# Optimization experiments

Measured on AMD Instinct MI355X. Metric: run time of the kernel, lower is better.

Reference implementation:

```python
import jax, jax.numpy as jnp
import numpy as np

GAMMA = 1.0
N_EXPERTS = 16
K = 8                      # number of trees (units of every Dense)
DEPTH = 4                  # log2(N_EXPERTS)
B, D_IN, D_OUT = 8192, 1024, 1024


def smoothstep(v):
    # 0 if v<=-g/2 ; 1 if v>=g/2 ; -2/g^3 v^3 + 3/(2g) v + 0.5 otherwise
    g = GAMMA
    poly = (-2.0 / g**3) * v**3 + (3.0 / (2.0 * g)) * v + 0.5
    return jnp.where(v <= -g / 2, 0.0, jnp.where(v >= g / 2, 1.0, poly))


def setup_inputs() -> dict:
    key = jax.random.key(0)
    ks = jax.random.split(key, 7)
    f = jax.random.normal(ks[0], (B, D_OUT, N_EXPERTS), jnp.float32)   # stacked experts
    x = jax.random.normal(ks[1], (B, D_IN), jnp.float32)               # routing inputs
    permutation_weights = jax.random.uniform(ks[2], (K, N_EXPERTS, N_EXPERTS), jnp.float32)
    zlo, zhi = -GAMMA / 100, GAMMA / 100                               # z_initializer range
    Wz = jax.random.uniform(ks[3], (N_EXPERTS - 1, D_IN, K), jnp.float32, zlo, zhi)
    bz = jax.random.uniform(ks[4], (N_EXPERTS - 1, K), jnp.float32, zlo, zhi)
    Ww = jax.random.uniform(ks[5], (N_EXPERTS, D_IN, K), jnp.float32)  # w_initializer U(0,1)
    bw = jax.random.uniform(ks[6], (N_EXPERTS, K), jnp.float32)
    return {"f": f, "x": x, "permutation_weights": permutation_weights,
            "Wz": Wz, "bz": bz, "Ww": Ww, "bw": bw}


def reference(f, x, permutation_weights, Wz, bz, Ww, bw):
    b = x.shape[0]
    # selector activations for all internal nodes (BFS order): [B, N_EXPERTS-1, K]
    s = smoothstep(jnp.einsum('bd,ndk->bnk', x, Wz) + bz)
    # propagate path probabilities level by level down the complete binary tree
    prob = jnp.ones((b, 1, K), x.dtype)
    for level in range(DEPTH):
        start = 2**level - 1
        p = s[:, start:start + 2**level, :]               # [B, 2^level, K]
        # left child gets prob*p, right child gets prob*(1-p)
        prob = jnp.stack([prob * p, prob * (1.0 - p)], axis=2).reshape(b, 2**(level + 1), K)
    # leaf dense outputs: [B, N_EXPERTS, K]
    a = jnp.einsum('bd,ndk->bnk', x, Ww) + bw
    log_prob = jnp.where(prob <= 0.0, jnp.finfo(jnp.float32).min, jnp.log(prob + 1e-8))
    s_bj = jnp.swapaxes(a + log_prob, 1, 2)               # [B, K, N_EXPERTS] (leaf order)
    g = jax.nn.softmax(s_bj.reshape(b, K * N_EXPERTS), axis=-1)
    g = g.reshape(b, 1, K, N_EXPERTS)                     # [B, 1, K, N]
    g_perm = jnp.einsum('bijk,jkl->bijl', g, permutation_weights)
    g_perm = jnp.sum(g_perm, axis=2, keepdims=True)       # [B, 1, 1, N]
    g_perm = g_perm / jnp.sum(g_perm, axis=-1, keepdims=True)
    # y = sum_n f[:, :, n] * g[:, n]  -> [B, D_OUT]
    y = jnp.einsum('bdn,bn->bd', f, g_perm[:, 0, 0, :])
    return y
```

## Files before the change

kernel.cpp:

```cpp
#include <hip/hip_runtime.h>
#include <hip/hip_bf16.h>
#include <math.h>

#define B_ROWS 8192
#define D_IN 1024
#define D_OUT 1024
#define NEXP 16
#define KDIM 8
#define NCOL 256

__global__ void wt_pack_kernel(const float* __restrict__ Wz,
                               const float* __restrict__ Ww,
                               float* __restrict__ Wt) {
    int d = blockIdx.x;
    int col = threadIdx.x;
    float v = 0.0f;
    if (col < 120) {
        int n = col >> 3, k = col & 7;
        v = Wz[n * (D_IN * 8) + d * 8 + k];
    } else if (col < 248) {
        int c = col - 120;
        int n = c >> 3, k = c & 7;
        v = Ww[n * (D_IN * 8) + d * 8 + k];
    }
    Wt[d * NCOL + col] = v;
}

#define BM 64
#define BN 64
#define KC 16
__global__ __launch_bounds__(256) void gemm_kernel(const float* __restrict__ x,
                                                   const float* __restrict__ Wt,
                                                   float* __restrict__ ZA) {
    __shared__ float xs[KC][BM];
    __shared__ float wsh[KC][BN];

    const int tid = threadIdx.x;
    const int bRow = blockIdx.x;
    const int bCol = blockIdx.y;
    const int tr = tid >> 4;
    const int tc = tid & 15;

    const int lxRow = tid >> 2;
    const int lxK = (tid & 3) << 2;
    const int lwK = tid >> 4;
    const int lwC = (tid & 15) << 2;

    const float* xg = x + (bRow * BM + lxRow) * D_IN + lxK;
    const float* wg = Wt + lwK * NCOL + bCol * BN + lwC;

    float4 px = *(const float4*)xg;
    float4 pw = *(const float4*)wg;

    float acc[4][4];
#pragma unroll
    for (int i = 0; i < 4; ++i)
#pragma unroll
        for (int j = 0; j < 4; ++j) acc[i][j] = 0.0f;

    for (int kc = 0; kc < D_IN; kc += KC) {
        xs[lxK + 0][lxRow] = px.x;
        xs[lxK + 1][lxRow] = px.y;
        xs[lxK + 2][lxRow] = px.z;
        xs[lxK + 3][lxRow] = px.w;
        *(float4*)&wsh[lwK][lwC] = pw;
        __syncthreads();
        if (kc + KC < D_IN) {
            px = *(const float4*)(xg + kc + KC);
            pw = *(const float4*)(wg + (kc + KC) * NCOL);
        }
#pragma unroll
        for (int kk = 0; kk < KC; ++kk) {
            const float4 xa = *(const float4*)&xs[kk][tr << 2];
            const float4 wv = *(const float4*)&wsh[kk][tc << 2];
            const float xr[4] = {xa.x, xa.y, xa.z, xa.w};
            const float wc[4] = {wv.x, wv.y, wv.z, wv.w};
#pragma unroll
            for (int i = 0; i < 4; ++i)
#pragma unroll
                for (int j = 0; j < 4; ++j) acc[i][j] += xr[i] * wc[j];
        }
        __syncthreads();
    }

    const int row0 = bRow * BM + (tr << 2);
    const int col0 = bCol * BN + (tc << 2);
#pragma unroll
    for (int i = 0; i < 4; ++i) {
        float4 o;
        o.x = acc[i][0]; o.y = acc[i][1]; o.z = acc[i][2]; o.w = acc[i][3];
        *(float4*)&ZA[(row0 + i) * NCOL + col0] = o;
    }
}

__global__ __launch_bounds__(128) void gate_kernel(const float* __restrict__ ZA,
                                                   const float* __restrict__ bz,
                                                   const float* __restrict__ bw,
                                                   const float* __restrict__ perm,
                                                   float* __restrict__ wout) {
    __shared__ float red[128];
    __shared__ float u[128];

    const int b = blockIdx.x;
    const int tid = threadIdx.x;
    const int kk = tid >> 4;
    const int n = tid & 15;

    const float* za = ZA + b * NCOL;

    float prob = 1.0f;
#pragma unroll
    for (int L = 0; L < 4; ++L) {
        const int node = (1 << L) - 1 + (n >> (4 - L));
        const int bit = (n >> (3 - L)) & 1;
        const float v = za[node * 8 + kk] + bz[node * 8 + kk];
        float p;
        if (v <= -0.5f) p = 0.0f;
        else if (v >= 0.5f) p = 1.0f;
        else p = fmaf(-2.0f * v * v, v, fmaf(1.5f, v, 0.5f));
        prob *= bit ? (1.0f - p) : p;
    }

    const float a = za[120 + n * 8 + kk] + bw[n * 8 + kk];
    const float logit = (prob <= 0.0f) ? -3.4e38f : (a + logf(prob + 1e-8f));

    red[tid] = logit;
    __syncthreads();
#pragma unroll
    for (int s = 64; s > 0; s >>= 1) {
        if (tid < s) red[tid] = fmaxf(red[tid], red[tid + s]);
        __syncthreads();
    }
    const float mx = red[0];
    __syncthreads();

    u[tid] = expf(logit - mx);
    __syncthreads();

    const int l = tid & 15;
    const int chunk = tid >> 4;
    float partial = 0.0f;
#pragma unroll
    for (int e0 = 0; e0 < 16; ++e0) {
        const int e = chunk * 16 + e0;
        partial += u[e] * perm[(e >> 4) * 256 + (e & 15) * 16 + l];
    }
    red[tid] = partial;
    __syncthreads();
#pragma unroll
    for (int s = 64; s >= 16; s >>= 1) {
        if (tid < s) red[tid] += red[tid + s];
        __syncthreads();
    }
    if (tid < 16) {
        float tot = 0.0f;
#pragma unroll
        for (int l2 = 0; l2 < 16; ++l2) tot += red[l2];
        wout[b * NEXP + tid] = red[tid] / tot;
    }
}

__global__ __launch_bounds__(256) void out_kernel(const float* __restrict__ f,
                                                  const float* __restrict__ w,
                                                  float* __restrict__ y) {
    __shared__ float ws_[16];
    const int b = blockIdx.x >> 2;
    const int d = ((blockIdx.x & 3) << 8) + threadIdx.x;
    if (threadIdx.x < 16) ws_[threadIdx.x] = w[b * NEXP + threadIdx.x];
    __syncthreads();

    const long idx = (long)b * D_OUT + d;
    const float4* f4 = (const float4*)(f + idx * NEXP);
    const float4 a0 = f4[0];
    const float4 a1 = f4[1];
    const float4 a2 = f4[2];
    const float4 a3 = f4[3];

    float r = a0.x * ws_[0] + a0.y * ws_[1] + a0.z * ws_[2] + a0.w * ws_[3]
            + a1.x * ws_[4] + a1.y * ws_[5] + a1.z * ws_[6] + a1.w * ws_[7]
            + a2.x * ws_[8] + a2.y * ws_[9] + a2.z * ws_[10] + a2.w * ws_[11]
            + a3.x * ws_[12] + a3.y * ws_[13] + a3.z * ws_[14] + a3.w * ws_[15];
    y[idx] = r;
}

extern "C" void kernel_launch(void* const* d_in, const int* in_sizes, int n_in,
                              void* d_out, int out_size, void* d_ws, size_t ws_size,
                              hipStream_t stream) {
    const float* f = (const float*)d_in[0];
    const float* x = (const float*)d_in[1];
    const float* perm = (const float*)d_in[2];
    const float* Wz = (const float*)d_in[3];
    const float* bz = (const float*)d_in[4];
    const float* Ww = (const float*)d_in[5];
    const float* bw = (const float*)d_in[6];
    float* y = (float*)d_out;

    float* Wt = (float*)d_ws;
    float* ZA = Wt + D_IN * NCOL;
    float* Wexp = ZA + B_ROWS * NCOL;

    wt_pack_kernel<<<dim3(D_IN), dim3(NCOL), 0, stream>>>(Wz, Ww, Wt);
    gemm_kernel<<<dim3(B_ROWS / BM, NCOL / BN), dim3(256), 0, stream>>>(x, Wt, ZA);
    gate_kernel<<<dim3(B_ROWS), dim3(128), 0, stream>>>(ZA, bz, bw, perm, Wexp);
    out_kernel<<<dim3(B_ROWS * 4), dim3(256), 0, stream>>>(f, Wexp, y);
}
```

Before: 779.6 us.

## Use split-bf16 MFMA for routing GEMM with transposed weight packing

Replaces the scalar FP32 SIMT GEMM with matrix-core MFMA 16x16x32 bf16 instructions, emulating FP32 accuracy by splitting each operand into high and low bf16 parts and summing three products. The weight pack kernel now writes a K-major transposed layout so both operands load contiguous along the reduction dimension. The aim is to cut the GEMM's compute time, at the cost of in-kernel conversion work and slightly reduced precision from dropping the low-low term.

```diff
diff --git a/kernel.cpp b/kernel.cpp
--- a/kernel.cpp
+++ b/kernel.cpp
@@ -1,5 +1,4 @@
 #include <hip/hip_runtime.h>
-#include <hip/hip_bf16.h>
 #include <math.h>
 
 #define B_ROWS 8192
@@ -9,88 +8,111 @@
 #define KDIM 8
 #define NCOL 256
 
-__global__ void wt_pack_kernel(const float* __restrict__ Wz,
-                               const float* __restrict__ Ww,
-                               float* __restrict__ Wt) {
-    int d = blockIdx.x;
-    int col = threadIdx.x;
-    float v = 0.0f;
-    if (col < 120) {
-        int n = col >> 3, k = col & 7;
-        v = Wz[n * (D_IN * 8) + d * 8 + k];
-    } else if (col < 248) {
-        int c = col - 120;
-        int n = c >> 3, k = c & 7;
-        v = Ww[n * (D_IN * 8) + d * 8 + k];
-    }
-    Wt[d * NCOL + col] = v;
+typedef __attribute__((ext_vector_type(8))) short bf16x8;
+typedef __attribute__((ext_vector_type(4))) float f32x4;
+
+__device__ __forceinline__ unsigned short f2bf_rne(float v) {
+    unsigned u = __float_as_uint(v);
+    u += 0x7fffu + ((u >> 16) & 1u);
+    return (unsigned short)(u >> 16);
+}
+__device__ __forceinline__ float bf2f(unsigned short h) {
+    return __uint_as_float(((unsigned)h) << 16);
+}
+
+__global__ __launch_bounds__(256) void wt_pack_kernel(const float* __restrict__ Wz,
+                                                      const float* __restrict__ Ww,
+                                                      float* __restrict__ WtT) {
+    const int c = blockIdx.x;
+    for (int d = threadIdx.x; d < D_IN; d += 256) {
+        float v = 0.0f;
+        if (c < 120) {
+            const int n = c >> 3, k = c & 7;
+            v = Wz[n * (D_IN * KDIM) + d * KDIM + k];
+        } else if (c < 248) {
+            const int cc = c - 120;
+            const int n = cc >> 3, k = cc & 7;
+            v = Ww[n * (D_IN * KDIM) + d * KDIM + k];
+        }
+        WtT[c * D_IN + d] = v;
+    }
 }
 
 #define BM 64
 #define BN 64
-#define KC 16
+#define KB 32
+
 __global__ __launch_bounds__(256) void gemm_kernel(const float* __restrict__ x,
-                                                   const float* __restrict__ Wt,
+                                                   const float* __restrict__ WtT,
                                                    float* __restrict__ ZA) {
-    __shared__ float xs[KC][BM];
-    __shared__ float wsh[KC][BN];
+    __shared__ bf16x8 XH[256], XL[256], WH[256], WL[256];
 
     const int tid = threadIdx.x;
-    const int bRow = blockIdx.x;
-    const int bCol = blockIdx.y;
-    const int tr = tid >> 4;
-    const int tc = tid & 15;
-
-    const int lxRow = tid >> 2;
-    const int lxK = (tid & 3) << 2;
-    const int lwK = tid >> 4;
-    const int lwC = (tid & 15) << 2;
-
-    const float* xg = x + (bRow * BM + lxRow) * D_IN + lxK;
-    const float* wg = Wt + lwK * NCOL + bCol * BN + lwC;
-
-    float4 px = *(const float4*)xg;
-    float4 pw = *(const float4*)wg;
-
-    float acc[4][4];
-#pragma unroll
-    for (int i = 0; i < 4; ++i)
-#pragma unroll
-        for (int j = 0; j < 4; ++j) acc[i][j] = 0.0f;
-
-    for (int kc = 0; kc < D_IN; kc += KC) {
-        xs[lxK + 0][lxRow] = px.x;
-        xs[lxK + 1][lxRow] = px.y;
-        xs[lxK + 2][lxRow] = px.z;
-        xs[lxK + 3][lxRow] = px.w;
-        *(float4*)&wsh[lwK][lwC] = pw;
-        __syncthreads();
-        if (kc + KC < D_IN) {
-            px = *(const float4*)(xg + kc + KC);
-            pw = *(const float4*)(wg + (kc + KC) * NCOL);
-        }
-#pragma unroll
-        for (int kk = 0; kk < KC; ++kk) {
-            const float4 xa = *(const float4*)&xs[kk][tr << 2];
-            const float4 wv = *(const float4*)&wsh[kk][tc << 2];
-            const float xr[4] = {xa.x, xa.y, xa.z, xa.w};
-            const float wc[4] = {wv.x, wv.y, wv.z, wv.w};
-#pragma unroll
-            for (int i = 0; i < 4; ++i)
-#pragma unroll
-                for (int j = 0; j < 4; ++j) acc[i][j] += xr[i] * wc[j];
-        }
-        __syncthreads();
-    }
-
-    const int row0 = bRow * BM + (tr << 2);
-    const int col0 = bCol * BN + (tc << 2);
-#pragma unroll
-    for (int i = 0; i < 4; ++i) {
-        float4 o;
-        o.x = acc[i][0]; o.y = acc[i][1]; o.z = acc[i][2]; o.w = acc[i][3];
-        *(float4*)&ZA[(row0 + i) * NCOL + col0] = o;
-    }
+    const int wave = tid >> 6;
+    const int lane = tid & 63;
+    const int rowBase = blockIdx.x * BM;
+    const int colBase = blockIdx.y * BN;
+
+    const int sRow = tid >> 2;
+    const int sKg = tid & 3;
+    const float* xg = x + (size_t)(rowBase + sRow) * D_IN + sKg * 8;
+    const float* wg = WtT + (size_t)(colBase + sRow) * D_IN + sKg * 8;
+    const int sUnit = ((sRow >> 4) << 6) | (sKg << 4) | (sRow & 15);
+
+    f32x4 acc[4];
+#pragma unroll
+    for (int ct = 0; ct < 4; ++ct)
+#pragma unroll
+        for (int q = 0; q < 4; ++q) acc[ct][q] = 0.0f;
+
+    float4 px0 = *(const float4*)(xg + 0);
+    float4 px1 = *(const float4*)(xg + 4);
+    float4 pw0 = *(const float4*)(wg + 0);
+    float4 pw1 = *(const float4*)(wg + 4);
+
+    for (int kk = 0; kk < D_IN; kk += KB) {
+        const float xv[8] = {px0.x, px0.y, px0.z, px0.w, px1.x, px1.y, px1.z, px1.w};
+        const float wv[8] = {pw0.x, pw0.y, pw0.z, pw0.w, pw1.x, pw1.y, pw1.z, pw1.w};
+        bf16x8 xh, xl, wh, wl;
+#pragma unroll
+        for (int i = 0; i < 8; ++i) {
+            unsigned short h = f2bf_rne(xv[i]);
+            xh[i] = (short)h;
+            xl[i] = (short)f2bf_rne(xv[i] - bf2f(h));
+            h = f2bf_rne(wv[i]);
+            wh[i] = (short)h;
+            wl[i] = (short)f2bf_rne(wv[i] - bf2f(h));
+        }
+        XH[sUnit] = xh; XL[sUnit] = xl; WH[sUnit] = wh; WL[sUnit] = wl;
+        __syncthreads();
+
+        if (kk + KB < D_IN) {
+            px0 = *(const float4*)(xg + kk + KB);
+            px1 = *(const float4*)(xg + kk + KB + 4);
+            pw0 = *(const float4*)(wg + kk + KB);
+            pw1 = *(const float4*)(wg + kk + KB + 4);
+        }
+
+        const bf16x8 ah = XH[(wave << 6) | lane];
+        const bf16x8 al = XL[(wave << 6) | lane];
+#pragma unroll
+        for (int ct = 0; ct < 4; ++ct) {
+            const bf16x8 bh = WH[(ct << 6) | lane];
+            const bf16x8 bl = WL[(ct << 6) | lane];
+            acc[ct] = __builtin_amdgcn_mfma_f32_16x16x32_bf16(ah, bh, acc[ct], 0, 0, 0);
+            acc[ct] = __builtin_amdgcn_mfma_f32_16x16x32_bf16(ah, bl, acc[ct], 0, 0, 0);
+            acc[ct] = __builtin_amdgcn_mfma_f32_16x16x32_bf16(al, bh, acc[ct], 0, 0, 0);
+        }
+        __syncthreads();
+    }
+
+    const int cRow = rowBase + wave * 16 + ((lane >> 4) << 2);
+    const int cCol = colBase + (lane & 15);
+#pragma unroll
+    for (int ct = 0; ct < 4; ++ct)
+#pragma unroll
+        for (int q = 0; q < 4; ++q)
+            ZA[(size_t)(cRow + q) * NCOL + cCol + ct * 16] = acc[ct][q];
 }
 
 __global__ __launch_bounds__(128) void gate_kernel(const float* __restrict__ ZA,
@@ -195,12 +217,12 @@
     const float* bw = (const float*)d_in[6];
     float* y = (float*)d_out;
 
-    float* Wt = (float*)d_ws;
-    float* ZA = Wt + D_IN * NCOL;
-    float* Wexp = ZA + B_ROWS * NCOL;
-
-    wt_pack_kernel<<<dim3(D_IN), dim3(NCOL), 0, stream>>>(Wz, Ww, Wt);
-    gemm_kernel<<<dim3(B_ROWS / BM, NCOL / BN), dim3(256), 0, stream>>>(x, Wt, ZA);
+    float* WtT = (float*)d_ws;
+    float* ZA = WtT + NCOL * D_IN;
+    float* Wexp = ZA + (size_t)B_ROWS * NCOL;
+
+    wt_pack_kernel<<<dim3(NCOL), dim3(256), 0, stream>>>(Wz, Ww, WtT);
+    gemm_kernel<<<dim3(B_ROWS / BM, NCOL / BN), dim3(256), 0, stream>>>(x, WtT, ZA);
     gate_kernel<<<dim3(B_ROWS), dim3(128), 0, stream>>>(ZA, bz, bw, perm, Wexp);
     out_kernel<<<dim3(B_ROWS * 4), dim3(256), 0, stream>>>(f, Wexp, y);
 }
```

Result: faster. 763.5 us (-2.1%).
